# Kernel optimization log

Hardware: AMD Instinct MI355X
Metric: run time of the kernel (lower is better)

## Reference

```python
import jax, jax.numpy as jnp
import numpy as np

B, C, FRAMES, E, W = 8, 2, 3999, 512, 16
STEP = W // 2  # frame_step = W//2 = 8


def setup_inputs() -> dict:
    key = jax.random.key(0)
    k1, k2 = jax.random.split(key)
    dec_input = jax.random.normal(k1, (B, C, FRAMES, E), dtype=jnp.float32)
    weight = jax.random.normal(k2, (W, E), dtype=jnp.float32) * (1.0 / np.sqrt(E))
    return {"dec_input": dec_input, "weight": weight}


def overlap_and_add(signal, frame_step):
    # signal: [..., frames, frame_length] -> [..., (frames-1)*step + frame_length]
    frames, frame_length = signal.shape[-2], signal.shape[-1]
    output_size = frame_step * (frames - 1) + frame_length
    # target sample index of every element of `signal`
    idx = (jnp.arange(frames)[:, None] * frame_step
           + jnp.arange(frame_length)[None, :]).reshape(-1)  # [frames*frame_length]
    flat = signal.reshape(*signal.shape[:-2], frames * frame_length)
    out = jnp.zeros((*signal.shape[:-2], output_size), dtype=signal.dtype)
    # scatter-accumulate overlapping frames along the last axis
    return out.at[..., idx].add(flat)


def reference(dec_input, weight):
    # dec_input: [B, C, frames, E]; weight: [W, E] (nn.Linear(E, W, bias=False))
    est_source = jnp.einsum('bcle,we->bclw', dec_input, weight)  # [B, C, frames, W]
    return overlap_and_add(est_source, STEP)  # [B, C, T]
```

## Files before the change

kernel.cpp:

```cpp
#include <hip/hip_runtime.h>
#include <cstdint>
#include <cstddef>


#define NBC     16
#define FRAMES  3999
#define EE      512
#define TOUT    32000
#define NGROUP  4000
#define GPB     63

__global__ __launch_bounds__(256, 4) void decoder_kernel(
    const float* __restrict__ dec,
    const float* __restrict__ wgt,
    float* __restrict__ out)
{
    __shared__ float smem[16 * EE];
    float* wl  = smem;
    float* red = smem;

    const int tid   = threadIdx.x;
    const int bc    = blockIdx.x >> 6;
    const int chunk = blockIdx.x & 63;
    const int g0    = chunk * GPB;

    {
        const float4* ws = (const float4*)wgt;
        float4*       wd = (float4*)wl;
        #pragma unroll
        for (int i = 0; i < 8; ++i)
            wd[tid + 256 * i] = ws[tid + 256 * i];
    }
    __syncthreads();

    const int s = tid & 63;
    const int q = tid >> 6;
    const int f = g0 - 1 + s;
    const float vmask = (f >= 0 && f < FRAMES) ? 1.0f : 0.0f;
    const int fr = min(max(f, 0), FRAMES - 1);

    const float* arow = dec + ((size_t)bc * FRAMES + fr) * EE + q * 128;
    const float* wbase = wl + q * 128;

    float acc[16];
    #pragma unroll
    for (int w = 0; w < 16; ++w) acc[w] = 0.f;

    #pragma unroll
    for (int c = 0; c < 8; ++c) {
        float4 xv[4];
        #pragma unroll
        for (int u = 0; u < 4; ++u)
            xv[u] = *(const float4*)(arow + c * 16 + 4 * u);

        #pragma unroll
        for (int w = 0; w < 16; ++w) {
            const float4* wrow = (const float4*)(wbase + w * EE + c * 16);
            float sum = 0.f;
            #pragma unroll
            for (int u = 0; u < 4; ++u) {
                const float4 wq = wrow[u];
                sum += xv[u].x * wq.x + xv[u].y * wq.y
                     + xv[u].z * wq.z + xv[u].w * wq.w;
            }
            acc[w] += sum;
        }
    }

    __syncthreads();
    #pragma unroll
    for (int w = 0; w < 16; ++w)
        red[(q * 16 + w) * 64 + s] = acc[w] * vmask;
    __syncthreads();

    for (int o = tid; o < GPB * 8; o += 256) {
        const int j = o >> 3;
        const int i = o & 7;
        const int g = g0 + j;
        if (g < NGROUP) {
            float v = 0.f;
            #pragma unroll
            for (int qq = 0; qq < 4; ++qq)
                v += red[(qq * 16 + i) * 64 + (j + 1)]
                   + red[(qq * 16 + 8 + i) * 64 + j];
            out[(size_t)bc * TOUT + g * 8 + i] = v;
        }
    }
}

extern "C" void kernel_launch(void* const* d_in, const int* in_sizes, int n_in,
                              void* d_out, int out_size, void* d_ws, size_t ws_size,
                              hipStream_t stream) {
    const float* dec = (const float*)d_in[0];
    const float* wgt = (const float*)d_in[1];
    float* out = (float*)d_out;

    decoder_kernel<<<dim3(1024), dim3(256), 0, stream>>>(dec, wgt, out);
}
```

Before: 196.8 us.

## Read weights directly via wave-uniform scalar loads instead of staging in LDS

```diff
diff --git a/kernel.cpp b/kernel.cpp
--- a/kernel.cpp
+++ b/kernel.cpp
@@ -10,41 +10,31 @@
 #define NGROUP  4000
 #define GPB     63
 
-__global__ __launch_bounds__(256, 4) void decoder_kernel(
+__global__ __launch_bounds__(256, 6) void decoder_kernel(
     const float* __restrict__ dec,
     const float* __restrict__ wgt,
     float* __restrict__ out)
 {
-    __shared__ float smem[16 * EE];
-    float* wl  = smem;
-    float* red = smem;
+    __shared__ float red[4 * 16 * 64];
 
     const int tid   = threadIdx.x;
     const int bc    = blockIdx.x >> 6;
     const int chunk = blockIdx.x & 63;
     const int g0    = chunk * GPB;
 
-    {
-        const float4* ws = (const float4*)wgt;
-        float4*       wd = (float4*)wl;
-        #pragma unroll
-        for (int i = 0; i < 8; ++i)
-            wd[tid + 256 * i] = ws[tid + 256 * i];
-    }
-    __syncthreads();
+    const int s = tid & 63;
+    const int q = __builtin_amdgcn_readfirstlane(tid >> 6);
 
-    const int s = tid & 63;
-    const int q = tid >> 6;
     const int f = g0 - 1 + s;
     const float vmask = (f >= 0 && f < FRAMES) ? 1.0f : 0.0f;
     const int fr = min(max(f, 0), FRAMES - 1);
 
-    const float* arow = dec + ((size_t)bc * FRAMES + fr) * EE + q * 128;
-    const float* wbase = wl + q * 128;
+    const float* arow  = dec + ((size_t)bc * FRAMES + fr) * EE + q * 128;
+    const float* wbase = wgt + q * 128;
 
-    float acc[16];
+    float2 acc[16];
     #pragma unroll
-    for (int w = 0; w < 16; ++w) acc[w] = 0.f;
+    for (int w = 0; w < 16; ++w) acc[w] = make_float2(0.f, 0.f);
 
     #pragma unroll
     for (int c = 0; c < 8; ++c) {
@@ -55,22 +45,21 @@
 
         #pragma unroll
         for (int w = 0; w < 16; ++w) {
-            const float4* wrow = (const float4*)(wbase + w * EE + c * 16);
-            float sum = 0.f;
+            const float* wr = wbase + w * EE + c * 16;
             #pragma unroll
             for (int u = 0; u < 4; ++u) {
-                const float4 wq = wrow[u];
-                sum += xv[u].x * wq.x + xv[u].y * wq.y
-                     + xv[u].z * wq.z + xv[u].w * wq.w;
+                const float4 wq = *(const float4*)(wr + 4 * u);
+                acc[w].x = fmaf(xv[u].x, wq.x, acc[w].x);
+                acc[w].y = fmaf(xv[u].y, wq.y, acc[w].y);
+                acc[w].x = fmaf(xv[u].z, wq.z, acc[w].x);
+                acc[w].y = fmaf(xv[u].w, wq.w, acc[w].y);
             }
-            acc[w] += sum;
         }
     }
 
-    __syncthreads();
     #pragma unroll
     for (int w = 0; w < 16; ++w)
-        red[(q * 16 + w) * 64 + s] = acc[w] * vmask;
+        red[(q * 16 + w) * 64 + s] = (acc[w].x + acc[w].y) * vmask;
     __syncthreads();
 
     for (int o = tid; o < GPB * 8; o += 256) {
```

Measured after the change: 201.5 us. +2.4%, slower.
